# Kernel optimization log

Measured on AMD Instinct MI355X. Metric: run time of the kernel, lower is better.

## Reference

```python
import jax, jax.numpy as jnp
import numpy as np

T, B, S, V, D = 64, 32, 400, 32000, 1536  # timesteps, batch, post len, vocab, dh+2*eh


def setup_inputs() -> dict:
    key = jax.random.key(0)
    k0, k1, k2, k3, k4 = jax.random.split(key, 5)
    return {
        "h": jax.random.normal(k0, (T, B, D), jnp.float32),
        "W": jax.random.normal(k1, (D, V), jnp.float32) * 0.02,
        "b": jnp.zeros((V,), jnp.float32),
        # attention weights over post positions (rows sum to 1, like the model's softmax attention)
        "att": jax.nn.softmax(jax.random.normal(k2, (T, B, S), jnp.float32), axis=-1),
        # generation probability in (0,1)
        "p_gen": jax.nn.sigmoid(jax.random.normal(k3, (T, B, 1), jnp.float32)),
        # post token ids, seq-first (S, B) as in the original data layout
        "post": jax.random.randint(k4, (S, B), 0, V),
    }


def reference(h, W, b, att, p_gen, post):
    # gen.w = wLinearLayer(gen.h): (T,B,D) @ (D,V) + (V,)
    w = jnp.einsum('tbd,dv->tbv', h, W) + b
    # sum_on_voc_index: scatter-add att[t,b,s] into voc_att[t,b,post[s,b]].
    # (The torch code builds a dense (B,V,S) zero buffer, scatter_'s the same
    # positions every timestep and sums over S -- identical to this scatter-add.)
    idx = post.T                                   # (B, S)
    b_idx = jnp.arange(B)[:, None]                 # (B, 1) -> broadcasts with idx
    voc_att = jnp.zeros((T, B, V), w.dtype).at[:, b_idx, idx].add(att)
    # pointer-generator mixture
    return p_gen * w + (1.0 - p_gen) * voc_att
```

## Files before the change

### kernel.cpp

```cpp
#include <hip/hip_runtime.h>
#include <hip/hip_bf16.h>
#include <stdint.h>

#define T_DIM 64
#define B_DIM 32
#define S_DIM 400
#define V_DIM 32000
#define D_DIM 1536
#define M_DIM (T_DIM * B_DIM)

typedef __attribute__((ext_vector_type(8))) short bf16x8;
typedef __attribute__((ext_vector_type(4))) float f32x4;

#define MEMFENCE asm volatile("" ::: "memory")
#define BARRIER() do { MEMFENCE; __builtin_amdgcn_s_barrier(); MEMFENCE; } while (0)


static __device__ __forceinline__ unsigned short f2bf(float x) {
    union { float f; uint32_t u; } v; v.f = x;
    uint32_t r = (v.u + 0x7FFFu + ((v.u >> 16) & 1u)) >> 16;
    return (unsigned short)r;
}

static __device__ __forceinline__ void gload_lds16(const void* g, void* l) {
    __builtin_amdgcn_global_load_lds(
        (const __attribute__((address_space(1))) uint32_t*)g,
        (__attribute__((address_space(3))) uint32_t*)l,
        16, 0, 0);
}


__global__ void convert_h(const float* __restrict__ h, unsigned short* __restrict__ hb) {
    const size_t n4 = (size_t)M_DIM * D_DIM / 4;
    for (size_t i = (size_t)blockIdx.x * blockDim.x + threadIdx.x; i < n4;
         i += (size_t)gridDim.x * blockDim.x) {
        const float4 v = ((const float4*)h)[i];
        ushort4 o;
        o.x = f2bf(v.x); o.y = f2bf(v.y); o.z = f2bf(v.z); o.w = f2bf(v.w);
        ((ushort4*)hb)[i] = o;
    }
}


__global__ __launch_bounds__(256)
void convT_W(const float* __restrict__ W, unsigned short* __restrict__ Wt) {
    __shared__ unsigned short lds[64 * 66];
    const int k0 = blockIdx.x * 64;
    const int v0 = blockIdx.y * 64;
    const int tid = threadIdx.x;
    const int rr = tid >> 4;
    const int cc = (tid & 15) * 4;

    #pragma unroll
    for (int p = 0; p < 4; ++p) {
        const int r = p * 16 + rr;
        const float4 v = *(const float4*)&W[(size_t)(k0 + r) * V_DIM + v0 + cc];
        unsigned short* q = &lds[r * 66 + cc];
        q[0] = f2bf(v.x); q[1] = f2bf(v.y); q[2] = f2bf(v.z); q[3] = f2bf(v.w);
    }
    __syncthreads();
    #pragma unroll
    for (int p = 0; p < 4; ++p) {
        const int n = p * 16 + rr;
        ushort4 o;
        o.x = lds[(cc + 0) * 66 + n];
        o.y = lds[(cc + 1) * 66 + n];
        o.z = lds[(cc + 2) * 66 + n];
        o.w = lds[(cc + 3) * 66 + n];
        *(ushort4*)&Wt[(size_t)(v0 + n) * D_DIM + k0 + cc] = o;
    }
}


#define BM3 256
#define BN3 256
#define BK3 64
#define NKT3 (D_DIM / BK3)

__global__ __launch_bounds__(512, 2)
void gemm_8phase(const unsigned short* __restrict__ A,
                 const unsigned short* __restrict__ Bt,
                 const float* __restrict__ bias,
                 const float* __restrict__ p_gen,
                 float* __restrict__ out) {
    __shared__ char lds[163840];

    const int bid = blockIdx.x;
    const int swz = (bid & 7) * 125 + (bid >> 3);
    const int m0 = (swz & 7) * BM3;
    const int n0 = (swz >> 3) * BN3;

    const int tid = threadIdx.x;
    const int lane = tid & 63;
    const int wid = tid >> 6;
    const int wr = wid >> 2;
    const int wc = wid & 3;
    const int rq = lane & 15;
    const int kq = lane >> 4;

    int stO[2], stRow[2], stCol[2];
    #pragma unroll
    for (int j = 0; j < 2; ++j) {
        const int o = tid * 16 + j * 8192;
        stO[j] = o;
        stRow[j] = o >> 7;
        stCol[j] = (o & 127) ^ (((o >> 7) & 7) << 4);
    }

    auto stageA = [&](int t, int half) {
        char* dst = lds + (t & 1) * 32768 + half * 16384;
        #pragma unroll
        for (int j = 0; j < 2; ++j) {
            const char* src = (const char*)A
                + (size_t)(m0 + half * 128 + stRow[j]) * (D_DIM * 2)
                + t * (BK3 * 2) + stCol[j];
            gload_lds16(src, dst + stO[j]);
        }
    };
    auto stageB = [&](int t, int half) {
        char* dst = lds + 65536 + (t % 3) * 32768 + half * 16384;
        #pragma unroll
        for (int j = 0; j < 2; ++j) {
            const char* src = (const char*)Bt
                + (size_t)(n0 + half * 128 + stRow[j]) * (D_DIM * 2)
                + t * (BK3 * 2) + stCol[j];
            gload_lds16(src, dst + stO[j]);
        }
    };

    int aOff[2][2][4], bOff[2][4];
    #pragma unroll
    for (int ks = 0; ks < 2; ++ks) {
        const int kb = ks * 64 + kq * 16;
        #pragma unroll
        for (int mh = 0; mh < 2; ++mh)
            #pragma unroll
            for (int mi = 0; mi < 4; ++mi) {
                const int row = wr * 128 + mh * 64 + mi * 16 + rq;
                aOff[ks][mh][mi] = row * 128 + (kb ^ ((row & 7) << 4));
            }
        #pragma unroll
        for (int nj = 0; nj < 4; ++nj) {
            const int row = wc * 64 + nj * 16 + rq;
            bOff[ks][nj] = row * 128 + (kb ^ ((row & 7) << 4));
        }
    }

    f32x4 acc[8][4] = {};
    bf16x8 aF[4], bF[4];

    stageA(0, 0); stageA(0, 1);
    stageB(0, 0); stageB(0, 1);
    stageB(1, 0); stageB(1, 1);

    for (int t = 0; t < NKT3; ++t) {
        const char* bufA = lds + (t & 1) * 32768;
        const char* bufB = lds + 65536 + (t % 3) * 32768;

        if (t == NKT3 - 1) { asm volatile("s_waitcnt vmcnt(0)" ::: "memory"); }
        else               { asm volatile("s_waitcnt vmcnt(4)" ::: "memory"); }

        #pragma unroll
        for (int ph = 0; ph < 4; ++ph) {
            const int ks = ph >> 1;
            const int mh = ph & 1;

            BARRIER();
            #pragma unroll
            for (int i = 0; i < 4; ++i)
                aF[i] = *(const bf16x8*)(bufA + aOff[ks][mh][i]);
            if (mh == 0) {
                #pragma unroll
                for (int nj = 0; nj < 4; ++nj)
                    bF[nj] = *(const bf16x8*)(bufB + bOff[ks][nj]);
            }
            if (ph < 2)      { if (t + 1 < NKT3) stageA(t + 1, ph); }
            else             { if (t + 2 < NKT3) stageB(t + 2, ph - 2); }

            __builtin_amdgcn_s_setprio(1);
            #pragma unroll
            for (int i = 0; i < 4; ++i)
                #pragma unroll
                for (int nj = 0; nj < 4; ++nj)
                    acc[mh * 4 + i][nj] = __builtin_amdgcn_mfma_f32_16x16x32_bf16(
                        aF[i], bF[nj], acc[mh * 4 + i][nj], 0, 0, 0);
            __builtin_amdgcn_s_setprio(0);
            BARRIER();
        }
    }

    const int rr4 = (lane >> 4) * 4;
    #pragma unroll
    for (int mi = 0; mi < 8; ++mi) {
        #pragma unroll
        for (int r = 0; r < 4; ++r) {
            const int m = m0 + wr * 128 + (mi >> 2) * 64 + (mi & 3) * 16 + rr4 + r;
            const float pgv = p_gen[m];
            #pragma unroll
            for (int nj = 0; nj < 4; ++nj) {
                const int n = n0 + wc * 64 + nj * 16 + rq;
                out[(size_t)m * V_DIM + n] = pgv * (acc[mi][nj][r] + bias[n]);
            }
        }
    }
}


__global__ void scatter_att(const float* __restrict__ att, const float* __restrict__ p_gen,
                            const int* __restrict__ post, float* __restrict__ out) {
    const int tb = blockIdx.x;
    const int b = tb & (B_DIM - 1);
    const float g = 1.0f - p_gen[tb];
    float* o = out + (size_t)tb * V_DIM;
    const float* a = att + (size_t)tb * S_DIM;
    for (int s = threadIdx.x; s < S_DIM; s += blockDim.x) {
        atomicAdd(&o[post[s * B_DIM + b]], g * a[s]);
    }
}


#define FB_MT 16
__global__ __launch_bounds__(256)
void gemm_naive(const float* __restrict__ h, const float* __restrict__ W,
                const float* __restrict__ bias, const float* __restrict__ pg,
                float* __restrict__ out) {
    const int mb = blockIdx.y;
    const int v = blockIdx.x * 256 + threadIdx.x;
    __shared__ float hs[FB_MT][128];
    float acc[FB_MT] = {};
    for (int k0 = 0; k0 < D_DIM; k0 += 128) {
        for (int i = threadIdx.x; i < FB_MT * 128; i += 256)
            hs[i >> 7][i & 127] = h[(size_t)(mb * FB_MT + (i >> 7)) * D_DIM + k0 + (i & 127)];
        __syncthreads();
        for (int kk = 0; kk < 128; ++kk) {
            const float wv = W[(size_t)(k0 + kk) * V_DIM + v];
            #pragma unroll
            for (int i = 0; i < FB_MT; ++i) acc[i] += hs[i][kk] * wv;
        }
        __syncthreads();
    }
    #pragma unroll
    for (int i = 0; i < FB_MT; ++i) {
        const int m = mb * FB_MT + i;
        out[(size_t)m * V_DIM + v] = pg[m] * (acc[i] + bias[v]);
    }
}


extern "C" void kernel_launch(void* const* d_in, const int* in_sizes, int n_in,
                              void* d_out, int out_size, void* d_ws, size_t ws_size,
                              hipStream_t stream) {
    const float* h    = (const float*)d_in[0];
    const float* W    = (const float*)d_in[1];
    const float* bias = (const float*)d_in[2];
    const float* att  = (const float*)d_in[3];
    const float* pg   = (const float*)d_in[4];
    const int*   post = (const int*)d_in[5];
    float* out = (float*)d_out;

    const size_t wt_bytes = (size_t)V_DIM * D_DIM * 2;
    const size_t hb_bytes = (size_t)M_DIM * D_DIM * 2;

    if (ws_size >= wt_bytes + hb_bytes) {
        unsigned short* Wt = (unsigned short*)d_ws;
        unsigned short* hb = (unsigned short*)((char*)d_ws + wt_bytes);
        convert_h<<<1024, 256, 0, stream>>>(h, hb);
        dim3 tg(D_DIM / 64, V_DIM / 64);
        convT_W<<<tg, 256, 0, stream>>>(W, Wt);
        gemm_8phase<<<(M_DIM / BM3) * (V_DIM / BN3), 512, 0, stream>>>(hb, Wt, bias, pg, out);
    } else {
        dim3 fg(V_DIM / 256, M_DIM / FB_MT);
        gemm_naive<<<fg, 256, 0, stream>>>(h, W, bias, pg, out);
    }

    scatter_att<<<M_DIM, 256, 0, stream>>>(att, pg, post, out);
}
```

Measured before the change: 332.8 us.

## Switch GEMM to 32x32x16 MFMA and fold h conversion into W transpose kernel

The GEMM inner loop now uses 32x32x16 bf16 MFMA tiles instead of 16x16x32. Each wave computes a 4x2 grid of 32x32 accumulators, with new LDS fragment offsets and an epilogue matching the 32x32 output layout. The larger tiles halve the number of MFMA issues and the LDS fragment reads per FLOP. Separately, the standalone h-to-bf16 conversion kernel is merged into the W transpose/convert kernel as a grid-stride loop, which saves one kernel launch. In exchange, the epilogue's row pattern makes global stores less contiguous.

Measured after the change: 348.1 us. 1.05x slower.

```diff
diff --git a/kernel.cpp b/kernel.cpp
--- a/kernel.cpp
+++ b/kernel.cpp
@@ -11,6 +11,7 @@
 
 typedef __attribute__((ext_vector_type(8))) short bf16x8;
 typedef __attribute__((ext_vector_type(4))) float f32x4;
+typedef __attribute__((ext_vector_type(16))) float f32x16;
 
 #define MEMFENCE asm volatile("" ::: "memory")
 #define BARRIER() do { MEMFENCE; __builtin_amdgcn_s_barrier(); MEMFENCE; } while (0)
@@ -30,26 +31,27 @@
 }
 
 
-__global__ void convert_h(const float* __restrict__ h, unsigned short* __restrict__ hb) {
-    const size_t n4 = (size_t)M_DIM * D_DIM / 4;
-    for (size_t i = (size_t)blockIdx.x * blockDim.x + threadIdx.x; i < n4;
-         i += (size_t)gridDim.x * blockDim.x) {
-        const float4 v = ((const float4*)h)[i];
-        ushort4 o;
-        o.x = f2bf(v.x); o.y = f2bf(v.y); o.z = f2bf(v.z); o.w = f2bf(v.w);
-        ((ushort4*)hb)[i] = o;
-    }
-}
-
-
 __global__ __launch_bounds__(256)
-void convT_W(const float* __restrict__ W, unsigned short* __restrict__ Wt) {
+void convT_W_h(const float* __restrict__ W, unsigned short* __restrict__ Wt,
+               const float* __restrict__ h, unsigned short* __restrict__ hb) {
     __shared__ unsigned short lds[64 * 66];
     const int k0 = blockIdx.x * 64;
     const int v0 = blockIdx.y * 64;
     const int tid = threadIdx.x;
     const int rr = tid >> 4;
     const int cc = (tid & 15) * 4;
+
+    {
+        const int nblk = gridDim.x * gridDim.y;
+        const int bidl = blockIdx.y * gridDim.x + blockIdx.x;
+        const size_t n4 = (size_t)M_DIM * D_DIM / 4;
+        for (size_t i = (size_t)bidl * 256 + tid; i < n4; i += (size_t)nblk * 256) {
+            const float4 v = ((const float4*)h)[i];
+            ushort4 o;
+            o.x = f2bf(v.x); o.y = f2bf(v.y); o.z = f2bf(v.z); o.w = f2bf(v.w);
+            ((ushort4*)hb)[i] = o;
+        }
+    }
 
     #pragma unroll
     for (int p = 0; p < 4; ++p) {
@@ -78,11 +80,11 @@
 #define NKT3 (D_DIM / BK3)
 
 __global__ __launch_bounds__(512, 2)
-void gemm_8phase(const unsigned short* __restrict__ A,
-                 const unsigned short* __restrict__ Bt,
-                 const float* __restrict__ bias,
-                 const float* __restrict__ p_gen,
-                 float* __restrict__ out) {
+void gemm_32x32(const unsigned short* __restrict__ A,
+                const unsigned short* __restrict__ Bt,
+                const float* __restrict__ bias,
+                const float* __restrict__ p_gen,
+                float* __restrict__ out) {
     __shared__ char lds[163840];
 
     const int bid = blockIdx.x;
@@ -95,8 +97,8 @@
     const int wid = tid >> 6;
     const int wr = wid >> 2;
     const int wc = wid & 3;
-    const int rq = lane & 15;
-    const int kq = lane >> 4;
+    const int l31 = lane & 31;
+    const int l5 = lane >> 5;
 
     int stO[2], stRow[2], stCol[2];
     #pragma unroll
@@ -128,26 +130,23 @@
         }
     };
 
-    int aOff[2][2][4], bOff[2][4];
-    #pragma unroll
-    for (int ks = 0; ks < 2; ++ks) {
-        const int kb = ks * 64 + kq * 16;
-        #pragma unroll
-        for (int mh = 0; mh < 2; ++mh)
-            #pragma unroll
-            for (int mi = 0; mi < 4; ++mi) {
-                const int row = wr * 128 + mh * 64 + mi * 16 + rq;
-                aOff[ks][mh][mi] = row * 128 + (kb ^ ((row & 7) << 4));
-            }
-        #pragma unroll
-        for (int nj = 0; nj < 4; ++nj) {
-            const int row = wc * 64 + nj * 16 + rq;
+    int aOff[4][4], bOff[4][2];
+    #pragma unroll
+    for (int ks = 0; ks < 4; ++ks) {
+        const int kb = ks * 32 + l5 * 16;
+        #pragma unroll
+        for (int mi = 0; mi < 4; ++mi) {
+            const int row = wr * 128 + mi * 32 + l31;
+            aOff[ks][mi] = row * 128 + (kb ^ ((row & 7) << 4));
+        }
+        #pragma unroll
+        for (int nj = 0; nj < 2; ++nj) {
+            const int row = wc * 64 + nj * 32 + l31;
             bOff[ks][nj] = row * 128 + (kb ^ ((row & 7) << 4));
         }
     }
 
-    f32x4 acc[8][4] = {};
-    bf16x8 aF[4], bF[4];
+    f32x16 acc[4][2] = {};
 
     stageA(0, 0); stageA(0, 1);
     stageB(0, 0); stageB(0, 1);
@@ -161,44 +160,40 @@
         else               { asm volatile("s_waitcnt vmcnt(4)" ::: "memory"); }
 
         #pragma unroll
-        for (int ph = 0; ph < 4; ++ph) {
-            const int ks = ph >> 1;
-            const int mh = ph & 1;
-
+        for (int ks = 0; ks < 4; ++ks) {
             BARRIER();
-            #pragma unroll
-            for (int i = 0; i < 4; ++i)
-                aF[i] = *(const bf16x8*)(bufA + aOff[ks][mh][i]);
-            if (mh == 0) {
+            bf16x8 aF[4], bF[2];
+            #pragma unroll
+            for (int mi = 0; mi < 4; ++mi)
+                aF[mi] = *(const bf16x8*)(bufA + aOff[ks][mi]);
+            #pragma unroll
+            for (int nj = 0; nj < 2; ++nj)
+                bF[nj] = *(const bf16x8*)(bufB + bOff[ks][nj]);
+
+            if (ks < 2)      { if (t + 1 < NKT3) stageA(t + 1, ks); }
+            else             { if (t + 2 < NKT3) stageB(t + 2, ks - 2); }
+
+            __builtin_amdgcn_s_setprio(1);
+            #pragma unroll
+            for (int mi = 0; mi < 4; ++mi)
                 #pragma unroll
-                for (int nj = 0; nj < 4; ++nj)
-                    bF[nj] = *(const bf16x8*)(bufB + bOff[ks][nj]);
-            }
-            if (ph < 2)      { if (t + 1 < NKT3) stageA(t + 1, ph); }
-            else             { if (t + 2 < NKT3) stageB(t + 2, ph - 2); }
-
-            __builtin_amdgcn_s_setprio(1);
-            #pragma unroll
-            for (int i = 0; i < 4; ++i)
-                #pragma unroll
-                for (int nj = 0; nj < 4; ++nj)
-                    acc[mh * 4 + i][nj] = __builtin_amdgcn_mfma_f32_16x16x32_bf16(
-                        aF[i], bF[nj], acc[mh * 4 + i][nj], 0, 0, 0);
+                for (int nj = 0; nj < 2; ++nj)
+                    acc[mi][nj] = __builtin_amdgcn_mfma_f32_32x32x16_bf16(
+                        aF[mi], bF[nj], acc[mi][nj], 0, 0, 0);
             __builtin_amdgcn_s_setprio(0);
             BARRIER();
         }
     }
 
-    const int rr4 = (lane >> 4) * 4;
-    #pragma unroll
-    for (int mi = 0; mi < 8; ++mi) {
-        #pragma unroll
-        for (int r = 0; r < 4; ++r) {
-            const int m = m0 + wr * 128 + (mi >> 2) * 64 + (mi & 3) * 16 + rr4 + r;
+    #pragma unroll
+    for (int mi = 0; mi < 4; ++mi) {
+        #pragma unroll
+        for (int r = 0; r < 16; ++r) {
+            const int m = m0 + wr * 128 + mi * 32 + (r & 3) + 8 * (r >> 2) + 4 * l5;
             const float pgv = p_gen[m];
             #pragma unroll
-            for (int nj = 0; nj < 4; ++nj) {
-                const int n = n0 + wc * 64 + nj * 16 + rq;
+            for (int nj = 0; nj < 2; ++nj) {
+                const int n = n0 + wc * 64 + nj * 32 + l31;
                 out[(size_t)m * V_DIM + n] = pgv * (acc[mi][nj][r] + bias[n]);
             }
         }
@@ -264,10 +259,9 @@
     if (ws_size >= wt_bytes + hb_bytes) {
         unsigned short* Wt = (unsigned short*)d_ws;
         unsigned short* hb = (unsigned short*)((char*)d_ws + wt_bytes);
-        convert_h<<<1024, 256, 0, stream>>>(h, hb);
         dim3 tg(D_DIM / 64, V_DIM / 64);
-        convT_W<<<tg, 256, 0, stream>>>(W, Wt);
-        gemm_8phase<<<(M_DIM / BM3) * (V_DIM / BN3), 512, 0, stream>>>(hb, Wt, bias, pg, out);
+        convT_W_h<<<tg, 256, 0, stream>>>(W, Wt, h, hb);
+        gemm_32x32<<<(M_DIM / BM3) * (V_DIM / BN3), 512, 0, stream>>>(hb, Wt, bias, pg, out);
     } else {
         dim3 fg(V_DIM / 256, M_DIM / FB_MT);
         gemm_naive<<<fg, 256, 0, stream>>>(h, W, bias, pg, out);
```

## Fuse fp32-to-bf16 conversion and W transpose into GEMM register-staged loads

Applied to the files above, without the earlier changes.

Removes the separate h conversion and W transpose/convert kernels. The GEMM now loads fp32 h and W directly into registers, converts them to bf16 and writes swizzled tiles to LDS, double-buffering both operands. This avoids writing and re-reading bf16 copies of W and h in workspace. In exchange it gives up direct global-to-LDS loads, and the W loads are strided 4-byte column reads. Each tile is re-read by 8 M-blocks in fp32, and the conversion ALU work sits inside the MFMA loop.

New measurement: 473.8 us. 42.4% more time.

```diff
diff --git a/kernel.cpp b/kernel.cpp
--- a/kernel.cpp
+++ b/kernel.cpp
@@ -17,58 +17,8 @@
 
 
 static __device__ __forceinline__ unsigned short f2bf(float x) {
-    union { float f; uint32_t u; } v; v.f = x;
-    uint32_t r = (v.u + 0x7FFFu + ((v.u >> 16) & 1u)) >> 16;
-    return (unsigned short)r;
-}
-
-static __device__ __forceinline__ void gload_lds16(const void* g, void* l) {
-    __builtin_amdgcn_global_load_lds(
-        (const __attribute__((address_space(1))) uint32_t*)g,
-        (__attribute__((address_space(3))) uint32_t*)l,
-        16, 0, 0);
-}
-
-
-__global__ void convert_h(const float* __restrict__ h, unsigned short* __restrict__ hb) {
-    const size_t n4 = (size_t)M_DIM * D_DIM / 4;
-    for (size_t i = (size_t)blockIdx.x * blockDim.x + threadIdx.x; i < n4;
-         i += (size_t)gridDim.x * blockDim.x) {
-        const float4 v = ((const float4*)h)[i];
-        ushort4 o;
-        o.x = f2bf(v.x); o.y = f2bf(v.y); o.z = f2bf(v.z); o.w = f2bf(v.w);
-        ((ushort4*)hb)[i] = o;
-    }
-}
-
-
-__global__ __launch_bounds__(256)
-void convT_W(const float* __restrict__ W, unsigned short* __restrict__ Wt) {
-    __shared__ unsigned short lds[64 * 66];
-    const int k0 = blockIdx.x * 64;
-    const int v0 = blockIdx.y * 64;
-    const int tid = threadIdx.x;
-    const int rr = tid >> 4;
-    const int cc = (tid & 15) * 4;
-
-    #pragma unroll
-    for (int p = 0; p < 4; ++p) {
-        const int r = p * 16 + rr;
-        const float4 v = *(const float4*)&W[(size_t)(k0 + r) * V_DIM + v0 + cc];
-        unsigned short* q = &lds[r * 66 + cc];
-        q[0] = f2bf(v.x); q[1] = f2bf(v.y); q[2] = f2bf(v.z); q[3] = f2bf(v.w);
-    }
-    __syncthreads();
-    #pragma unroll
-    for (int p = 0; p < 4; ++p) {
-        const int n = p * 16 + rr;
-        ushort4 o;
-        o.x = lds[(cc + 0) * 66 + n];
-        o.y = lds[(cc + 1) * 66 + n];
-        o.z = lds[(cc + 2) * 66 + n];
-        o.w = lds[(cc + 3) * 66 + n];
-        *(ushort4*)&Wt[(size_t)(v0 + n) * D_DIM + k0 + cc] = o;
-    }
+    __hip_bfloat16 b = __float2bfloat16(x);
+    return *reinterpret_cast<unsigned short*>(&b);
 }
 
 
@@ -78,12 +28,12 @@
 #define NKT3 (D_DIM / BK3)
 
 __global__ __launch_bounds__(512, 2)
-void gemm_8phase(const unsigned short* __restrict__ A,
-                 const unsigned short* __restrict__ Bt,
-                 const float* __restrict__ bias,
-                 const float* __restrict__ p_gen,
-                 float* __restrict__ out) {
-    __shared__ char lds[163840];
+void gemm_fused(const float* __restrict__ h,
+                const float* __restrict__ W,
+                const float* __restrict__ bias,
+                const float* __restrict__ p_gen,
+                float* __restrict__ out) {
+    __shared__ char lds[131072];
 
     const int bid = blockIdx.x;
     const int swz = (bid & 7) * 125 + (bid >> 3);
@@ -98,33 +48,58 @@
     const int rq = lane & 15;
     const int kq = lane >> 4;
 
-    int stO[2], stRow[2], stCol[2];
+    const int srow = tid & 255;
+    const int kou = (tid >> 8) * 4;
+
+    const float* hrow = h + (size_t)(m0 + srow) * D_DIM;
+    const float* wcol = W + (n0 + srow);
+
+    int wOff[4];
     #pragma unroll
-    for (int j = 0; j < 2; ++j) {
-        const int o = tid * 16 + j * 8192;
-        stO[j] = o;
-        stRow[j] = o >> 7;
-        stCol[j] = (o & 127) ^ (((o >> 7) & 7) << 4);
-    }
-
-    auto stageA = [&](int t, int half) {
-        char* dst = lds + (t & 1) * 32768 + half * 16384;
-        #pragma unroll
-        for (int j = 0; j < 2; ++j) {
-            const char* src = (const char*)A
-                + (size_t)(m0 + half * 128 + stRow[j]) * (D_DIM * 2)
-                + t * (BK3 * 2) + stCol[j];
-            gload_lds16(src, dst + stO[j]);
-        }
-    };
-    auto stageB = [&](int t, int half) {
-        char* dst = lds + 65536 + (t % 3) * 32768 + half * 16384;
-        #pragma unroll
-        for (int j = 0; j < 2; ++j) {
-            const char* src = (const char*)Bt
-                + (size_t)(n0 + half * 128 + stRow[j]) * (D_DIM * 2)
-                + t * (BK3 * 2) + stCol[j];
-            gload_lds16(src, dst + stO[j]);
+    for (int u = 0; u < 4; ++u)
+        wOff[u] = srow * 128 + (((kou + u) * 16) ^ ((srow & 7) << 4));
+
+    float4 aS[8];
+    float bS[4][8];
+
+    auto issueA = [&](int t) {
+        const float* p = hrow + t * BK3;
+        #pragma unroll
+        for (int u = 0; u < 4; ++u) {
+            aS[u * 2 + 0] = *(const float4*)(p + (kou + u) * 8 + 0);
+            aS[u * 2 + 1] = *(const float4*)(p + (kou + u) * 8 + 4);
+        }
+    };
+    auto issueB2 = [&](int t, int u0) {
+        #pragma unroll
+        for (int uu = 0; uu < 2; ++uu) {
+            const int u = u0 + uu;
+            const float* p = wcol + (size_t)(t * BK3 + (kou + u) * 8) * V_DIM;
+            #pragma unroll
+            for (int j = 0; j < 8; ++j)
+                bS[u][j] = p[(size_t)j * V_DIM];
+        }
+    };
+    auto writeA = [&](int t) {
+        char* buf = lds + (t & 1) * 32768;
+        #pragma unroll
+        for (int u = 0; u < 4; ++u) {
+            union { bf16x8 v; unsigned short s[8]; } r;
+            const float* x0 = (const float*)&aS[u * 2 + 0];
+            const float* x1 = (const float*)&aS[u * 2 + 1];
+            #pragma unroll
+            for (int j = 0; j < 4; ++j) { r.s[j] = f2bf(x0[j]); r.s[4 + j] = f2bf(x1[j]); }
+            *(bf16x8*)(buf + wOff[u]) = r.v;
+        }
+    };
+    auto writeB = [&](int t) {
+        char* buf = lds + 65536 + (t & 1) * 32768;
+        #pragma unroll
+        for (int u = 0; u < 4; ++u) {
+            union { bf16x8 v; unsigned short s[8]; } r;
+            #pragma unroll
+            for (int j = 0; j < 8; ++j) r.s[j] = f2bf(bS[u][j]);
+            *(bf16x8*)(buf + wOff[u]) = r.v;
         }
     };
 
@@ -149,16 +124,15 @@
     f32x4 acc[8][4] = {};
     bf16x8 aF[4], bF[4];
 
-    stageA(0, 0); stageA(0, 1);
-    stageB(0, 0); stageB(0, 1);
-    stageB(1, 0); stageB(1, 1);
+    issueA(0); issueB2(0, 0); issueB2(0, 2);
+    writeA(0); writeB(0);
+    asm volatile("s_waitcnt lgkmcnt(0)" ::: "memory");
+    BARRIER();
 
     for (int t = 0; t < NKT3; ++t) {
         const char* bufA = lds + (t & 1) * 32768;
-        const char* bufB = lds + 65536 + (t % 3) * 32768;
-
-        if (t == NKT3 - 1) { asm volatile("s_waitcnt vmcnt(0)" ::: "memory"); }
-        else               { asm volatile("s_waitcnt vmcnt(4)" ::: "memory"); }
+        const char* bufB = lds + 65536 + (t & 1) * 32768;
+        const bool more = (t + 1 < NKT3);
 
         #pragma unroll
         for (int ph = 0; ph < 4; ++ph) {
@@ -174,8 +148,13 @@
                 for (int nj = 0; nj < 4; ++nj)
                     bF[nj] = *(const bf16x8*)(bufB + bOff[ks][nj]);
             }
-            if (ph < 2)      { if (t + 1 < NKT3) stageA(t + 1, ph); }
-            else             { if (t + 2 < NKT3) stageB(t + 2, ph - 2); }
+
+            if (more) {
+                if (ph == 0)      { issueA(t + 1); issueB2(t + 1, 0); }
+                else if (ph == 1) { issueB2(t + 1, 2); }
+                else if (ph == 2) { writeA(t + 1); }
+                else              { writeB(t + 1); }
+            }
 
             __builtin_amdgcn_s_setprio(1);
             #pragma unroll
@@ -185,6 +164,7 @@
                     acc[mh * 4 + i][nj] = __builtin_amdgcn_mfma_f32_16x16x32_bf16(
                         aF[i], bF[nj], acc[mh * 4 + i][nj], 0, 0, 0);
             __builtin_amdgcn_s_setprio(0);
+            if (ph == 3) asm volatile("s_waitcnt lgkmcnt(0)" ::: "memory");
             BARRIER();
         }
     }
@@ -215,34 +195,6 @@
     const float* a = att + (size_t)tb * S_DIM;
     for (int s = threadIdx.x; s < S_DIM; s += blockDim.x) {
         atomicAdd(&o[post[s * B_DIM + b]], g * a[s]);
-    }
-}
-
-
-#define FB_MT 16
-__global__ __launch_bounds__(256)
-void gemm_naive(const float* __restrict__ h, const float* __restrict__ W,
-                const float* __restrict__ bias, const float* __restrict__ pg,
-                float* __restrict__ out) {
-    const int mb = blockIdx.y;
-    const int v = blockIdx.x * 256 + threadIdx.x;
-    __shared__ float hs[FB_MT][128];
-    float acc[FB_MT] = {};
-    for (int k0 = 0; k0 < D_DIM; k0 += 128) {
-        for (int i = threadIdx.x; i < FB_MT * 128; i += 256)
-            hs[i >> 7][i & 127] = h[(size_t)(mb * FB_MT + (i >> 7)) * D_DIM + k0 + (i & 127)];
-        __syncthreads();
-        for (int kk = 0; kk < 128; ++kk) {
-            const float wv = W[(size_t)(k0 + kk) * V_DIM + v];
-            #pragma unroll
-            for (int i = 0; i < FB_MT; ++i) acc[i] += hs[i][kk] * wv;
-        }
-        __syncthreads();
-    }
-    #pragma unroll
-    for (int i = 0; i < FB_MT; ++i) {
-        const int m = mb * FB_MT + i;
-        out[(size_t)m * V_DIM + v] = pg[m] * (acc[i] + bias[v]);
     }
 }
 
@@ -258,20 +210,6 @@
     const int*   post = (const int*)d_in[5];
     float* out = (float*)d_out;
 
-    const size_t wt_bytes = (size_t)V_DIM * D_DIM * 2;
-    const size_t hb_bytes = (size_t)M_DIM * D_DIM * 2;
-
-    if (ws_size >= wt_bytes + hb_bytes) {
-        unsigned short* Wt = (unsigned short*)d_ws;
-        unsigned short* hb = (unsigned short*)((char*)d_ws + wt_bytes);
-        convert_h<<<1024, 256, 0, stream>>>(h, hb);
-        dim3 tg(D_DIM / 64, V_DIM / 64);
-        convT_W<<<tg, 256, 0, stream>>>(W, Wt);
-        gemm_8phase<<<(M_DIM / BM3) * (V_DIM / BN3), 512, 0, stream>>>(hb, Wt, bias, pg, out);
-    } else {
-        dim3 fg(V_DIM / 256, M_DIM / FB_MT);
-        gemm_naive<<<fg, 256, 0, stream>>>(h, W, bias, pg, out);
-    }
-
+    gemm_fused<<<(M_DIM / BM3) * (V_DIM / BN3), 512, 0, stream>>>(h, W, bias, pg, out);
     scatter_att<<<M_DIM, 256, 0, stream>>>(att, pg, post, out);
 }
```
